# Kernel optimization log

Hardware: AMD Instinct MI355X
Metric: run time of the kernel (lower is better)

The kernel has to match this reference:

```python
import jax, jax.numpy as jnp
import numpy as np

NUM_CLASSES = 6
GROUP = 256
TEMP = 2.0
LAM = 0.8  # soft_lambda mixing rotation vs translation label distance


def _rnc_core(feat, label_dist, t):
    # Rank-N-Contrast: for anchor i, positive j (j!=i), denominator over k with
    # label_dist[i,k] >= label_dist[i,j], k != i.  feat [n,d], label_dist [n,n].
    n = feat.shape[0]
    diff = feat[:, None, :] - feat[None, :, :]
    dist = jnp.sqrt(jnp.sum(diff * diff, axis=-1) + 1e-12)  # [n,n] l2 feature distance
    logits = -dist / t
    logits = logits - jax.lax.stop_gradient(jnp.max(logits, axis=1, keepdims=True))
    exp_logits = jnp.exp(logits)
    eye = jnp.eye(n, dtype=bool)
    # mask[i,j,k]: k belongs to the denominator set of anchor i / positive j
    mask = (label_dist[:, None, :] >= label_dist[:, :, None]) & (~eye)[:, None, :]
    denom = jnp.einsum('ijk,ik->ij', mask.astype(feat.dtype), exp_logits)  # [n,n]
    log_prob = logits - jnp.log(denom)
    return -jnp.sum(jnp.where(eye, 0.0, log_prob)) / (n * (n - 1))


def _l1_pair(x):
    # pairwise l1 distance summed over last dim: [n,n]
    return jnp.sum(jnp.abs(x[:, None, :] - x[None, :, :]), axis=-1)


def _loss_sym(feat, green, trans):
    L = LAM * _l1_pair(green) + (1.0 - LAM) * _l1_pair(trans)
    return _rnc_core(feat, L, TEMP)


def _loss_nonsym(feat, green, red, trans):
    rot = 0.5 * (_l1_pair(green) + _l1_pair(red))
    L = LAM * rot + (1.0 - LAM) * _l1_pair(trans)
    return _rnc_core(feat, L, TEMP)


def _loss_mug(feat, green, red, trans, sym):
    nonsym = (sym[:, 0] == 0).astype(feat.dtype)
    both = nonsym[:, None] * nonsym[None, :]  # red axis only matters when both non-sym
    rot = (_l1_pair(green) + both * _l1_pair(red)) / (1.0 + both)
    L = LAM * rot + (1.0 - LAM) * _l1_pair(trans)
    return _rnc_core(feat, L, TEMP)


def setup_inputs() -> dict:
    key = jax.random.key(0)
    ks = jax.random.split(key, 4)
    B = NUM_CLASSES * GROUP
    D = 256
    features = jax.random.normal(ks[0], (B, D), dtype=jnp.float32)
    labels = jnp.repeat(jnp.arange(NUM_CLASSES, dtype=jnp.int32), GROUP)

    def unit(k, shape):
        v = jax.random.normal(k, shape, dtype=jnp.float32)
        return v / jnp.linalg.norm(v, axis=-1, keepdims=True)

    gt_green = unit(ks[1], (B, 3))
    gt_red = unit(ks[2], (B, 3))
    gt_trans = jax.random.normal(ks[3], (B, 3), dtype=jnp.float32)
    # sym flags: classes 0,1 fully symmetric (sym[:,0]==1 everywhere -> rnc_loss);
    # classes 2,3,4 have sym[:,0]==0 -> nonSym branch; class 5 (mug) mixed flags.
    sym0 = np.ones((B,), dtype=np.int32)
    for c in (2, 3, 4):
        sym0[c * GROUP:(c + 1) * GROUP] = 0
    sym0[5 * GROUP:5 * GROUP + GROUP // 2] = 0
    sym = np.zeros((B, 4), dtype=np.int32)
    sym[:, 0] = sym0
    return {"features": features, "labels": labels, "gt_green": gt_green,
            "gt_red": gt_red, "gt_trans": gt_trans, "sym": jnp.asarray(sym)}


def reference(features, labels, gt_green, gt_red, gt_trans, sym):
    # labels are sorted into NUM_CLASSES equal contiguous groups of size GROUP,
    # so the per-unique-label gather becomes static slicing.
    total = jnp.float32(0.0)
    for c in range(NUM_CLASSES):
        s = slice(c * GROUP, (c + 1) * GROUP)
        f, g, r, t, sy = features[s], gt_green[s], gt_red[s], gt_trans[s], sym[s]
        if c == 5:
            total = total + _loss_mug(f, g, r, t, sy)
        elif c in (0, 1):  # no sym[:,0]==0 entries -> symmetric RnC loss
            total = total + _loss_sym(f, g, t)
        else:
            total = total + _loss_nonsym(f, g, r, t)
    return total / NUM_CLASSES
```

## Files before the change

### kernel.cpp

```cpp
#include <hip/hip_runtime.h>
#include <cmath>

#define NCLS 6
#define GRP 256
#define DIM 256
#define TA 4

__global__ __launch_bounds__(256) void transpose_kernel(
    const float* __restrict__ feat, float* __restrict__ ft)
{
    __shared__ float tile[64][65];
    const int b  = blockIdx.x;
    const int c  = b >> 4;
    const int tt = b & 15;
    const int r0 = (tt >> 2) << 6;
    const int c0 = (tt & 3) << 6;
    const int t  = threadIdx.x;

    #pragma unroll
    for (int q = 0; q < 4; ++q) {
        int idx  = q * 256 + t;
        int row  = idx >> 4;
        int col4 = (idx & 15) << 2;
        float4 v = *reinterpret_cast<const float4*>(
            feat + (size_t)(c * 256 + r0 + row) * DIM + c0 + col4);
        tile[row][col4 + 0] = v.x; tile[row][col4 + 1] = v.y;
        tile[row][col4 + 2] = v.z; tile[row][col4 + 3] = v.w;
    }
    __syncthreads();
    #pragma unroll
    for (int q = 0; q < 4; ++q) {
        int idx = q * 256 + t;
        int dd  = idx >> 4;
        int r4  = (idx & 15) << 2;
        float4 o = make_float4(tile[r4][dd], tile[r4 + 1][dd],
                               tile[r4 + 2][dd], tile[r4 + 3][dd]);
        *reinterpret_cast<float4*>(
            ft + (size_t)(c * 256 + c0 + dd) * GRP + r0 + r4) = o;
    }
}

__global__ __launch_bounds__(256) void rnc_main_kernel(
    const float* __restrict__ ft,
    const float* __restrict__ green,
    const float* __restrict__ red,
    const float* __restrict__ trans,
    const int*   __restrict__ sym,
    float* __restrict__ partial)
{
    __shared__ __align__(16) float4 fi4[DIM];
    __shared__ float dist_lds[TA][GRP + 1];
    __shared__ __align__(16) float2 LE[TA][258];

    const int b    = blockIdx.x;
    const int c    = b >> 6;
    const int a0   = (b & 63) << 2;
    const int base = c << 8;
    const int t    = threadIdx.x;

    fi4[t] = *reinterpret_cast<const float4*>(ft + (size_t)(c * 256 + t) * GRP + a0);
    __syncthreads();

    const float* cp = ft + (size_t)(c * 256) * GRP + t;
    float ac0 = 0.f, ac1 = 0.f, ac2 = 0.f, ac3 = 0.f;
    #pragma unroll 8
    for (int d = 0; d < DIM; ++d) {
        float v  = cp[(size_t)d * GRP];
        float4 f = fi4[d];
        float x;
        x = f.x - v; ac0 = fmaf(x, x, ac0);
        x = f.y - v; ac1 = fmaf(x, x, ac1);
        x = f.z - v; ac2 = fmaf(x, x, ac2);
        x = f.w - v; ac3 = fmaf(x, x, ac3);
    }
    dist_lds[0][t] = sqrtf(ac0 + 1e-12f);
    dist_lds[1][t] = sqrtf(ac1 + 1e-12f);
    dist_lds[2][t] = sqrtf(ac2 + 1e-12f);
    dist_lds[3][t] = sqrtf(ac3 + 1e-12f);
    __syncthreads();

    const int w  = t >> 6;
    const int l  = t & 63;
    const int iw = a0 + w;
    const int ag = base + iw;

    float dj0 = dist_lds[w][l];
    float dj1 = dist_lds[w][l + 64];
    float dj2 = dist_lds[w][l + 128];
    float dj3 = dist_lds[w][l + 192];

    float m = fminf(fminf(dj0, dj1), fminf(dj2, dj3));
    #pragma unroll
    for (int off = 32; off > 0; off >>= 1)
        m = fminf(m, __shfl_xor(m, off));
    const float dmin = m;

    {
        const float gx = green[3 * ag], gy = green[3 * ag + 1], gz = green[3 * ag + 2];
        const float tx = trans[3 * ag], ty = trans[3 * ag + 1], tz = trans[3 * ag + 2];
        float rx = 0.f, ry = 0.f, rz = 0.f;
        int syma = 0;
        if (c >= 2) { rx = red[3 * ag]; ry = red[3 * ag + 1]; rz = red[3 * ag + 2]; }
        if (c == 5) { syma = sym[4 * ag]; }

        float djv[4] = {dj0, dj1, dj2, dj3};
        #pragma unroll
        for (int jj = 0; jj < 4; ++jj) {
            const int j  = l + (jj << 6);
            const int kg = base + j;
            float l1g = fabsf(gx - green[3 * kg]) + fabsf(gy - green[3 * kg + 1])
                      + fabsf(gz - green[3 * kg + 2]);
            float l1t = fabsf(tx - trans[3 * kg]) + fabsf(ty - trans[3 * kg + 1])
                      + fabsf(tz - trans[3 * kg + 2]);
            float L;
            if (c < 2) {
                L = 0.8f * l1g + 0.2f * l1t;
            } else {
                float l1r = fabsf(rx - red[3 * kg]) + fabsf(ry - red[3 * kg + 1])
                          + fabsf(rz - red[3 * kg + 2]);
                float rot;
                if (c < 5) {
                    rot = 0.5f * (l1g + l1r);
                } else {
                    float both = ((syma == 0) && (sym[4 * kg] == 0)) ? 1.f : 0.f;
                    rot = (l1g + both * l1r) / (1.f + both);
                }
                L = 0.8f * rot + 0.2f * l1t;
            }
            float ev = __expf((dmin - djv[jj]) * 0.5f);
            LE[w][j] = make_float2(L, ev);
        }
    }
    __syncthreads();

    float L0, L1, L2, L3;
    L0 = LE[w][l].x; L1 = LE[w][l + 64].x; L2 = LE[w][l + 128].x; L3 = LE[w][l + 192].x;
    const float4* p4 = reinterpret_cast<const float4*>(&LE[w][0]);
    float dn0 = 0.f, dn1 = 0.f, dn2 = 0.f, dn3 = 0.f;
    #pragma unroll 4
    for (int q = 0; q < 64; ++q) {
        float4 u = p4[2 * q];
        float4 v = p4[2 * q + 1];
        dn0 += (u.x >= L0) ? u.y : 0.f;
        dn1 += (u.x >= L1) ? u.y : 0.f;
        dn2 += (u.x >= L2) ? u.y : 0.f;
        dn3 += (u.x >= L3) ? u.y : 0.f;
        dn0 += (u.z >= L0) ? u.w : 0.f;
        dn1 += (u.z >= L1) ? u.w : 0.f;
        dn2 += (u.z >= L2) ? u.w : 0.f;
        dn3 += (u.z >= L3) ? u.w : 0.f;
        dn0 += (v.x >= L0) ? v.y : 0.f;
        dn1 += (v.x >= L1) ? v.y : 0.f;
        dn2 += (v.x >= L2) ? v.y : 0.f;
        dn3 += (v.x >= L3) ? v.y : 0.f;
        dn0 += (v.z >= L0) ? v.w : 0.f;
        dn1 += (v.z >= L1) ? v.w : 0.f;
        dn2 += (v.z >= L2) ? v.w : 0.f;
        dn3 += (v.z >= L3) ? v.w : 0.f;
    }

    float part = 0.f;
    if (l + 0   != iw) part += (dmin - dj0) * 0.5f - __logf(dn0);
    if (l + 64  != iw) part += (dmin - dj1) * 0.5f - __logf(dn1);
    if (l + 128 != iw) part += (dmin - dj2) * 0.5f - __logf(dn2);
    if (l + 192 != iw) part += (dmin - dj3) * 0.5f - __logf(dn3);
    #pragma unroll
    for (int off = 32; off > 0; off >>= 1)
        part += __shfl_xor(part, off);
    if (l == 0) partial[ag] = part;
}

__global__ __launch_bounds__(256) void rnc_finalize_kernel(
    const float* __restrict__ partial, float* __restrict__ out)
{
    __shared__ float rbuf[4];
    int t = threadIdx.x;
    float acc = 0.f;
    for (int k = t; k < NCLS * GRP; k += 256) acc += partial[k];
    #pragma unroll
    for (int off = 32; off > 0; off >>= 1)
        acc += __shfl_down(acc, off);
    if ((t & 63) == 0) rbuf[t >> 6] = acc;
    __syncthreads();
    if (t == 0)
        out[0] = -(rbuf[0] + rbuf[1] + rbuf[2] + rbuf[3]) / (256.f * 255.f * 6.f);
}

extern "C" void kernel_launch(void* const* d_in, const int* in_sizes, int n_in,
                              void* d_out, int out_size, void* d_ws, size_t ws_size,
                              hipStream_t stream)
{
    const float* feat  = (const float*)d_in[0];
    const float* green = (const float*)d_in[2];
    const float* red   = (const float*)d_in[3];
    const float* trans = (const float*)d_in[4];
    const int*   sym   = (const int*)d_in[5];

    float* wsf     = (float*)d_ws;
    float* partial = wsf;
    float* ft      = wsf + 2048;
    float* out     = (float*)d_out;

    transpose_kernel<<<NCLS * 16, 256, 0, stream>>>(feat, ft);
    rnc_main_kernel<<<NCLS * (GRP / TA), 256, 0, stream>>>(ft, green, red, trans, sym, partial);
    rnc_finalize_kernel<<<1, 256, 0, stream>>>(partial, out);
}
```

Measured before the change: 34.79 us.

## Split RnC main kernel into distance/label and denominator kernels

Replaces the single fused kernel with two kernels. The first computes pairwise feature distances, splitting the feature dimension across two thread halves, and writes label distances plus logits for every anchor/candidate pair to a global float2 buffer. The second kernel runs one block per anchor and splits the denominator comparison loop across the four waves, finishing with an LDS reduction. This raises block count and cuts the per-thread serial work in the denominator stage, and it also drops the per-anchor max shift, which cancels mathematically in log_prob. The cost is an extra kernel launch and a few megabytes of intermediate global traffic.

```diff
diff --git a/kernel.cpp b/kernel.cpp
--- a/kernel.cpp
+++ b/kernel.cpp
@@ -4,7 +4,6 @@
 #define NCLS 6
 #define GRP 256
 #define DIM 256
-#define TA 4
 
 __global__ __launch_bounds__(256) void transpose_kernel(
     const float* __restrict__ feat, float* __restrict__ ft)
@@ -40,134 +39,136 @@
     }
 }
 
-__global__ __launch_bounds__(256) void rnc_main_kernel(
+__global__ __launch_bounds__(256) void dist_label_kernel(
+    const float* __restrict__ feat,
     const float* __restrict__ ft,
     const float* __restrict__ green,
     const float* __restrict__ red,
     const float* __restrict__ trans,
     const int*   __restrict__ sym,
-    float* __restrict__ partial)
-{
-    __shared__ __align__(16) float4 fi4[DIM];
-    __shared__ float dist_lds[TA][GRP + 1];
-    __shared__ __align__(16) float2 LE[TA][258];
-
-    const int b    = blockIdx.x;
-    const int c    = b >> 6;
-    const int a0   = (b & 63) << 2;
-    const int base = c << 8;
-    const int t    = threadIdx.x;
-
-    fi4[t] = *reinterpret_cast<const float4*>(ft + (size_t)(c * 256 + t) * GRP + a0);
-    __syncthreads();
-
-    const float* cp = ft + (size_t)(c * 256) * GRP + t;
+    float2* __restrict__ LE)
+{
+    __shared__ float part[2][4][128];
+
+    const int b   = blockIdx.x;
+    const int c   = b >> 7;
+    const int r   = b & 127;
+    const int q   = r >> 1;
+    const int h   = r & 1;
+    const int t   = threadIdx.x;
+    const int col = t & 127;
+    const int dh  = t >> 7;
+    const int a0g = (c << 8) + (q << 2);
+    const int k   = (h << 7) + col;
+    const int kg  = (c << 8) + k;
+
+    const float* f0 = feat + (size_t)a0g * DIM + (dh << 7);
+    const float* cp = ft + ((size_t)((c << 8) + (dh << 7))) * GRP + k;
+
     float ac0 = 0.f, ac1 = 0.f, ac2 = 0.f, ac3 = 0.f;
     #pragma unroll 8
-    for (int d = 0; d < DIM; ++d) {
-        float v  = cp[(size_t)d * GRP];
-        float4 f = fi4[d];
+    for (int d = 0; d < 128; ++d) {
+        float v = cp[(size_t)d * GRP];
         float x;
-        x = f.x - v; ac0 = fmaf(x, x, ac0);
-        x = f.y - v; ac1 = fmaf(x, x, ac1);
-        x = f.z - v; ac2 = fmaf(x, x, ac2);
-        x = f.w - v; ac3 = fmaf(x, x, ac3);
-    }
-    dist_lds[0][t] = sqrtf(ac0 + 1e-12f);
-    dist_lds[1][t] = sqrtf(ac1 + 1e-12f);
-    dist_lds[2][t] = sqrtf(ac2 + 1e-12f);
-    dist_lds[3][t] = sqrtf(ac3 + 1e-12f);
-    __syncthreads();
-
-    const int w  = t >> 6;
-    const int l  = t & 63;
-    const int iw = a0 + w;
-    const int ag = base + iw;
-
-    float dj0 = dist_lds[w][l];
-    float dj1 = dist_lds[w][l + 64];
-    float dj2 = dist_lds[w][l + 128];
-    float dj3 = dist_lds[w][l + 192];
-
-    float m = fminf(fminf(dj0, dj1), fminf(dj2, dj3));
-    #pragma unroll
-    for (int off = 32; off > 0; off >>= 1)
-        m = fminf(m, __shfl_xor(m, off));
-    const float dmin = m;
-
-    {
-        const float gx = green[3 * ag], gy = green[3 * ag + 1], gz = green[3 * ag + 2];
-        const float tx = trans[3 * ag], ty = trans[3 * ag + 1], tz = trans[3 * ag + 2];
-        float rx = 0.f, ry = 0.f, rz = 0.f;
-        int syma = 0;
-        if (c >= 2) { rx = red[3 * ag]; ry = red[3 * ag + 1]; rz = red[3 * ag + 2]; }
-        if (c == 5) { syma = sym[4 * ag]; }
-
-        float djv[4] = {dj0, dj1, dj2, dj3};
-        #pragma unroll
-        for (int jj = 0; jj < 4; ++jj) {
-            const int j  = l + (jj << 6);
-            const int kg = base + j;
-            float l1g = fabsf(gx - green[3 * kg]) + fabsf(gy - green[3 * kg + 1])
-                      + fabsf(gz - green[3 * kg + 2]);
-            float l1t = fabsf(tx - trans[3 * kg]) + fabsf(ty - trans[3 * kg + 1])
-                      + fabsf(tz - trans[3 * kg + 2]);
-            float L;
-            if (c < 2) {
-                L = 0.8f * l1g + 0.2f * l1t;
+        x = f0[d]       - v; ac0 = fmaf(x, x, ac0);
+        x = f0[256 + d] - v; ac1 = fmaf(x, x, ac1);
+        x = f0[512 + d] - v; ac2 = fmaf(x, x, ac2);
+        x = f0[768 + d] - v; ac3 = fmaf(x, x, ac3);
+    }
+    part[dh][0][col] = ac0; part[dh][1][col] = ac1;
+    part[dh][2][col] = ac2; part[dh][3][col] = ac3;
+    __syncthreads();
+
+    const int p = dh;
+    float s0 = part[0][p][col]     + part[1][p][col];
+    float s1 = part[0][p + 2][col] + part[1][p + 2][col];
+    float lg0 = -0.5f * sqrtf(s0 + 1e-12f);
+    float lg1 = -0.5f * sqrtf(s1 + 1e-12f);
+
+    float kgx = green[3 * kg], kgy = green[3 * kg + 1], kgz = green[3 * kg + 2];
+    float ktx = trans[3 * kg], kty = trans[3 * kg + 1], ktz = trans[3 * kg + 2];
+    float krx = 0.f, kry = 0.f, krz = 0.f;
+    int ksym = 0;
+    if (c >= 2) { krx = red[3 * kg]; kry = red[3 * kg + 1]; krz = red[3 * kg + 2]; }
+    if (c == 5) { ksym = sym[4 * kg]; }
+
+    #pragma unroll
+    for (int e = 0; e < 2; ++e) {
+        const int ag = a0g + p + 2 * e;
+        float l1g = fabsf(green[3*ag] - kgx) + fabsf(green[3*ag+1] - kgy)
+                  + fabsf(green[3*ag+2] - kgz);
+        float l1t = fabsf(trans[3*ag] - ktx) + fabsf(trans[3*ag+1] - kty)
+                  + fabsf(trans[3*ag+2] - ktz);
+        float L;
+        if (c < 2) {
+            L = 0.8f * l1g + 0.2f * l1t;
+        } else {
+            float l1r = fabsf(red[3*ag] - krx) + fabsf(red[3*ag+1] - kry)
+                      + fabsf(red[3*ag+2] - krz);
+            float rot;
+            if (c < 5) {
+                rot = 0.5f * (l1g + l1r);
             } else {
-                float l1r = fabsf(rx - red[3 * kg]) + fabsf(ry - red[3 * kg + 1])
-                          + fabsf(rz - red[3 * kg + 2]);
-                float rot;
-                if (c < 5) {
-                    rot = 0.5f * (l1g + l1r);
-                } else {
-                    float both = ((syma == 0) && (sym[4 * kg] == 0)) ? 1.f : 0.f;
-                    rot = (l1g + both * l1r) / (1.f + both);
-                }
-                L = 0.8f * rot + 0.2f * l1t;
+                float both = ((sym[4*ag] == 0) && (ksym == 0)) ? 1.f : 0.f;
+                rot = (l1g + both * l1r) / (1.f + both);
             }
-            float ev = __expf((dmin - djv[jj]) * 0.5f);
-            LE[w][j] = make_float2(L, ev);
+            L = 0.8f * rot + 0.2f * l1t;
         }
-    }
-    __syncthreads();
-
-    float L0, L1, L2, L3;
-    L0 = LE[w][l].x; L1 = LE[w][l + 64].x; L2 = LE[w][l + 128].x; L3 = LE[w][l + 192].x;
-    const float4* p4 = reinterpret_cast<const float4*>(&LE[w][0]);
+        LE[(size_t)ag * GRP + k] = make_float2(L, e == 0 ? lg0 : lg1);
+    }
+}
+
+__global__ __launch_bounds__(256) void denom_kernel(
+    const float2* __restrict__ LE,
+    float* __restrict__ partial)
+{
+    __shared__ __align__(16) float2 LEs[GRP];
+    __shared__ __align__(16) float pd[GRP][4];
+    __shared__ float rbuf[4];
+
+    const int a = blockIdx.x;
+    const int i = a & 255;
+    const int t = threadIdx.x;
+    const int w = t >> 6;
+    const int l = t & 63;
+
+    float2 g = LE[(size_t)a * GRP + t];
+    const float lgt = g.y;
+    LEs[t] = make_float2(g.x, __expf(g.y));
+    __syncthreads();
+
+    float L0 = LEs[l].x;
+    float L1 = LEs[l + 64].x;
+    float L2 = LEs[l + 128].x;
+    float L3 = LEs[l + 192].x;
+
+    const float4* p4 = reinterpret_cast<const float4*>(LEs);
     float dn0 = 0.f, dn1 = 0.f, dn2 = 0.f, dn3 = 0.f;
-    #pragma unroll 4
-    for (int q = 0; q < 64; ++q) {
-        float4 u = p4[2 * q];
-        float4 v = p4[2 * q + 1];
-        dn0 += (u.x >= L0) ? u.y : 0.f;
-        dn1 += (u.x >= L1) ? u.y : 0.f;
-        dn2 += (u.x >= L2) ? u.y : 0.f;
-        dn3 += (u.x >= L3) ? u.y : 0.f;
-        dn0 += (u.z >= L0) ? u.w : 0.f;
-        dn1 += (u.z >= L1) ? u.w : 0.f;
-        dn2 += (u.z >= L2) ? u.w : 0.f;
-        dn3 += (u.z >= L3) ? u.w : 0.f;
-        dn0 += (v.x >= L0) ? v.y : 0.f;
-        dn1 += (v.x >= L1) ? v.y : 0.f;
-        dn2 += (v.x >= L2) ? v.y : 0.f;
-        dn3 += (v.x >= L3) ? v.y : 0.f;
-        dn0 += (v.z >= L0) ? v.w : 0.f;
-        dn1 += (v.z >= L1) ? v.w : 0.f;
-        dn2 += (v.z >= L2) ? v.w : 0.f;
-        dn3 += (v.z >= L3) ? v.w : 0.f;
-    }
-
-    float part = 0.f;
-    if (l + 0   != iw) part += (dmin - dj0) * 0.5f - __logf(dn0);
-    if (l + 64  != iw) part += (dmin - dj1) * 0.5f - __logf(dn1);
-    if (l + 128 != iw) part += (dmin - dj2) * 0.5f - __logf(dn2);
-    if (l + 192 != iw) part += (dmin - dj3) * 0.5f - __logf(dn3);
+    const int q0 = w << 5;
+    #pragma unroll 8
+    for (int q = q0; q < q0 + 32; ++q) {
+        float4 u = p4[q];
+        dn0 += (u.x >= L0) ? u.y : 0.f;  dn0 += (u.z >= L0) ? u.w : 0.f;
+        dn1 += (u.x >= L1) ? u.y : 0.f;  dn1 += (u.z >= L1) ? u.w : 0.f;
+        dn2 += (u.x >= L2) ? u.y : 0.f;  dn2 += (u.z >= L2) ? u.w : 0.f;
+        dn3 += (u.x >= L3) ? u.y : 0.f;  dn3 += (u.z >= L3) ? u.w : 0.f;
+    }
+    pd[l][w]       = dn0;
+    pd[l + 64][w]  = dn1;
+    pd[l + 128][w] = dn2;
+    pd[l + 192][w] = dn3;
+    __syncthreads();
+
+    float4 dns = *reinterpret_cast<const float4*>(pd[t]);
+    float dn = (dns.x + dns.y) + (dns.z + dns.w);
+    float part = (t != i) ? (lgt - __logf(dn)) : 0.f;
+
     #pragma unroll
     for (int off = 32; off > 0; off >>= 1)
         part += __shfl_xor(part, off);
-    if (l == 0) partial[ag] = part;
+    if (l == 0) rbuf[w] = part;
+    __syncthreads();
+    if (t == 0) partial[a] = (rbuf[0] + rbuf[1]) + (rbuf[2] + rbuf[3]);
 }
 
 __global__ __launch_bounds__(256) void rnc_finalize_kernel(
@@ -196,12 +197,14 @@
     const float* trans = (const float*)d_in[4];
     const int*   sym   = (const int*)d_in[5];
 
-    float* wsf     = (float*)d_ws;
-    float* partial = wsf;
-    float* ft      = wsf + 2048;
-    float* out     = (float*)d_out;
+    float*  wsf     = (float*)d_ws;
+    float*  partial = wsf;
+    float*  ft      = wsf + 2048;
+    float2* LE      = (float2*)(wsf + 2048 + NCLS * GRP * DIM);
+    float*  out     = (float*)d_out;
 
     transpose_kernel<<<NCLS * 16, 256, 0, stream>>>(feat, ft);
-    rnc_main_kernel<<<NCLS * (GRP / TA), 256, 0, stream>>>(ft, green, red, trans, sym, partial);
+    dist_label_kernel<<<NCLS * 128, 256, 0, stream>>>(feat, ft, green, red, trans, sym, LE);
+    denom_kernel<<<NCLS * GRP, 256, 0, stream>>>(LE, partial);
     rnc_finalize_kernel<<<1, 256, 0, stream>>>(partial, out);
 }
```

New measurement: 41.04 us. +18.0%, slower.
